# Kernel tuning notes

Hardware: AMD Instinct MI355X
Metric: run time of the kernel (lower is better)

Reference implementation:

```python
import jax, jax.numpy as jnp
import numpy as np

# RosaAttention config constants
H = 16       # num_rosa_heads
KV = 4       # num_rosa_key_value_heads
QKB = 64     # num_rosa_query_key_bits
VB = 64      # num_rosa_value_bits
HID = 2048   # hidden_size
TAU = 1.0    # temperature buffer


def setup_inputs() -> dict:
    key = jax.random.key(0)
    ks = jax.random.split(key, 8)
    B, S = 2, 2048
    sc = 0.02
    return {
        "x": jax.random.normal(ks[0], (B, S, HID), jnp.float32),
        "attention_mask": jnp.ones((B, S), jnp.int32),
        "Wq": jax.random.normal(ks[1], (HID, H * QKB), jnp.float32) * sc,
        "Wk": jax.random.normal(ks[2], (HID, KV * QKB), jnp.float32) * sc,
        "Wv": jax.random.normal(ks[3], (HID, KV * VB), jnp.float32) * sc,
        "Wo": jax.random.normal(ks[4], (H * VB, HID), jnp.float32) * sc,
        "emb0": jnp.full((H, VB), -1e-05, jnp.float32),
        "emb1": jnp.full((H, VB), +1e-05, jnp.float32),
    }


def reference(x, attention_mask, Wq, Wk, Wv, Wo, emb0, emb1):
    B, S, _ = x.shape
    rep = H // KV
    # projections -> [b, s, heads, bits]
    xq = (x @ Wq).reshape(B, S, H, QKB)
    xk = (x @ Wk).reshape(B, S, KV, QKB)
    xv = (x @ Wv).reshape(B, S, KV, VB)
    # repeat_kv: each kv head repeated n_rep times contiguously
    xk = jnp.repeat(xk, rep, axis=2)   # [b, s, H, QKB]
    xv = jnp.repeat(xv, rep, axis=2)   # [b, s, H, VB]
    # soft bit quantization of q/k, tau-scaled bit-similarity score
    qb = jnp.tanh(xq)
    kb = jnp.tanh(xk)
    scores = jnp.einsum('bqhd,bkhd->bhqk', qb, kb) / (TAU * QKB)
    # causal mask + padding mask (mask True = attend)
    causal = jnp.tril(jnp.ones((S, S), bool))
    mask = causal[None, None] & attention_mask.astype(bool)[:, None, None, :]
    scores = jnp.where(mask, scores, jnp.finfo(scores.dtype).min)
    probs = jax.nn.softmax(scores, axis=-1)        # [b, h, q, k]
    # soft-binarized values: per-bit probabilities, attended, then mapped
    # through learned per-head bit embeddings emb0 (bit=0) / emb1 (bit=1)
    vp = jax.nn.sigmoid(xv)                        # [b, s, H, VB]
    ctx = jnp.einsum('bhqk,bkhv->bqhv', probs, vp) # [b, s, H, VB]
    out_bits = ctx * emb1[None, None] + (1.0 - ctx) * emb0[None, None]
    out = out_bits.reshape(B, S, H * VB) @ Wo      # [b, s, HID]
    return out
```

## Files before the change

kernel.cpp:

```cpp
#include <hip/hip_runtime.h>
#include <math.h>

typedef short bf16x8 __attribute__((ext_vector_type(8)));
typedef float f32x4 __attribute__((ext_vector_type(4)));

#define MFMA_BF16(A,B,C) __builtin_amdgcn_mfma_f32_16x16x32_bf16(A,B,C,0,0,0)

__device__ __forceinline__ unsigned short f2b(float x) {
    union { float f; unsigned int u; } v; v.f = x;
    unsigned int r = v.u + 0x7FFFu + ((v.u >> 16) & 1u);
    return (unsigned short)(r >> 16);
}

__device__ __forceinline__ void gload16(const unsigned short* g, unsigned short* l) {
    __builtin_amdgcn_global_load_lds(
        (const __attribute__((address_space(1))) unsigned int*)(g),
        (__attribute__((address_space(3))) unsigned int*)(l),
        16, 0, 0);
}
__device__ __forceinline__ void gload4(const int* g, int* l) {
    __builtin_amdgcn_global_load_lds(
        (const __attribute__((address_space(1))) unsigned int*)(g),
        (__attribute__((address_space(3))) unsigned int*)(l),
        4, 0, 0);
}

__global__ __launch_bounds__(256) void conv_bf16(const float* __restrict__ s,
                                                 unsigned short* __restrict__ d, int n)
{
    int i = blockIdx.x * blockDim.x + threadIdx.x;
    int stride = gridDim.x * blockDim.x;
    for (int idx = i * 4; idx < n; idx += stride * 4) {
        float4 v = *(const float4*)(s + idx);
        ushort4 o;
        o.x = f2b(v.x); o.y = f2b(v.y); o.z = f2b(v.z); o.w = f2b(v.w);
        *(ushort4*)(d + idx) = o;
    }
}

__global__ __launch_bounds__(256) void transp_conv_qkv(const float* __restrict__ Wq,
                                                       const float* __restrict__ Wk,
                                                       const float* __restrict__ Wv,
                                                       unsigned short* __restrict__ dst)
{
    __shared__ float t[32][33];
    const int tx = threadIdx.x, ty = threadIdx.y;
    int bx = blockIdx.x;
    const float* src; int C, cb, dco;
    if (bx < 32)      { src = Wq; C = 1024; cb = bx;      dco = 0; }
    else if (bx < 40) { src = Wk; C = 256;  cb = bx - 32; dco = 1024; }
    else              { src = Wv; C = 256;  cb = bx - 40; dco = 1280; }
    const int c = cb * 32 + tx;
    const int r0 = blockIdx.y * 32;
#pragma unroll
    for (int i = 0; i < 4; ++i)
        t[ty + i * 8][tx] = src[(size_t)(r0 + ty + i * 8) * C + c];
    __syncthreads();
    const int cc = cb * 32 + ty;
#pragma unroll
    for (int i = 0; i < 4; ++i)
        dst[(size_t)(dco + cc + i * 8) * 2048 + r0 + tx] = f2b(t[tx][ty + i * 8]);
}

__global__ __launch_bounds__(256) void transp_conv(const float* __restrict__ src, int R, int C,
                                                   unsigned short* __restrict__ dst, int pitch)
{
    __shared__ float t[32][33];
    const int tx = threadIdx.x, ty = threadIdx.y;
    const int c = blockIdx.x * 32 + tx;
    const int r0 = blockIdx.y * 32;
#pragma unroll
    for (int i = 0; i < 4; ++i)
        t[ty + i * 8][tx] = src[(size_t)(r0 + ty + i * 8) * C + c];
    __syncthreads();
    const int cc = blockIdx.x * 32 + ty;
#pragma unroll
    for (int i = 0; i < 4; ++i)
        dst[(size_t)(cc + i * 8) * pitch + r0 + tx] = f2b(t[tx][ty + i * 8]);
}

template <int MODE>
__global__ __launch_bounds__(256, 3) void gemm_bt_mfma(
    const unsigned short* __restrict__ A,
    const unsigned short* __restrict__ Bt,
    int M, int N, int K,
    float* __restrict__ Cf,
    unsigned short* __restrict__ qh,
    unsigned short* __restrict__ kh,
    unsigned short* __restrict__ vtt)
{
    __shared__ __align__(16) unsigned short As[2][2 * 128 * 32];
    __shared__ __align__(16) unsigned short Bs[2][2 * 64 * 32];

    const int tid = threadIdx.x;
    const int w = tid >> 6, lane = tid & 63, l15 = lane & 15, quad = lane >> 4;
    const int wm = w & 1, wn = w >> 1;
    const int m0 = blockIdx.y * 128, n0 = blockIdx.x * 64;

    f32x4 acc[4][2];
    const f32x4 zero4 = {0.f, 0.f, 0.f, 0.f};
#pragma unroll
    for (int i = 0; i < 4; ++i)
#pragma unroll
        for (int j = 0; j < 2; ++j) acc[i][j] = zero4;

    const int lrow = lane >> 2, lcol = (lane & 3) * 8;
    const unsigned short* AgL = A  + (size_t)(m0 + w * 32 + lrow) * K + lcol;
    const unsigned short* BgL = Bt + (size_t)(n0 + w * 16 + lrow) * K + lcol;

#pragma unroll
    for (int t = 0; t < 4; ++t) {
        const int sub = t >> 1, half = t & 1;
        gload16(AgL + (size_t)(half * 16) * K + sub * 32,
                &As[0][sub * 4096 + (w * 32 + half * 16) * 32]);
    }
#pragma unroll
    for (int kk = 0; kk < 2; ++kk)
        gload16(BgL + kk * 32, &Bs[0][kk * 2048 + (w * 16) * 32]);
    __syncthreads();

    int cb = 0;
    for (int k0 = 0; k0 < K; k0 += 64) {
        if (k0 + 64 < K) {
            const int nb = cb ^ 1;
#pragma unroll
            for (int t = 0; t < 4; ++t) {
                const int sub = t >> 1, half = t & 1;
                gload16(AgL + (size_t)(half * 16) * K + (k0 + 64) + sub * 32,
                        &As[nb][sub * 4096 + (w * 32 + half * 16) * 32]);
            }
#pragma unroll
            for (int kk = 0; kk < 2; ++kk)
                gload16(BgL + (k0 + 64) + kk * 32, &Bs[nb][kk * 2048 + (w * 16) * 32]);
        }

        bf16x8 af[4][2], bf[2][2];
#pragma unroll
        for (int kk = 0; kk < 2; ++kk) {
#pragma unroll
            for (int mt = 0; mt < 4; ++mt)
                af[mt][kk] = *(const bf16x8*)&As[cb][kk * 4096 + (wm * 64 + mt * 16 + l15) * 32 + quad * 8];
#pragma unroll
            for (int nt = 0; nt < 2; ++nt)
                bf[nt][kk] = *(const bf16x8*)&Bs[cb][kk * 2048 + (wn * 32 + nt * 16 + l15) * 32 + quad * 8];
        }
#pragma unroll
        for (int kk = 0; kk < 2; ++kk)
#pragma unroll
            for (int mt = 0; mt < 4; ++mt)
#pragma unroll
                for (int nt = 0; nt < 2; ++nt)
                    acc[mt][nt] = MFMA_BF16(af[mt][kk], bf[nt][kk], acc[mt][nt]);

        __syncthreads();
        cb ^= 1;
    }

    if (MODE == 0) {
#pragma unroll
        for (int mt = 0; mt < 4; ++mt)
#pragma unroll
            for (int nt = 0; nt < 2; ++nt) {
                const int gn = n0 + wn * 32 + nt * 16 + l15;
#pragma unroll
                for (int r = 0; r < 4; ++r) {
                    const int gm = m0 + wm * 64 + mt * 16 + quad * 4 + r;
                    Cf[(size_t)gm * N + gn] = acc[mt][nt][r];
                }
            }
    } else {
        if (n0 < 1024) {
#pragma unroll
            for (int mt = 0; mt < 4; ++mt)
#pragma unroll
                for (int nt = 0; nt < 2; ++nt) {
                    const int gn = n0 + wn * 32 + nt * 16 + l15;
#pragma unroll
                    for (int r = 0; r < 4; ++r) {
                        const int gm = m0 + wm * 64 + mt * 16 + quad * 4 + r;
                        qh[(size_t)gm * 1024 + gn] = f2b(tanhf(acc[mt][nt][r]));
                    }
                }
        } else if (n0 < 1280) {
#pragma unroll
            for (int mt = 0; mt < 4; ++mt)
#pragma unroll
                for (int nt = 0; nt < 2; ++nt) {
                    const int gn = n0 + wn * 32 + nt * 16 + l15 - 1024;
#pragma unroll
                    for (int r = 0; r < 4; ++r) {
                        const int gm = m0 + wm * 64 + mt * 16 + quad * 4 + r;
                        kh[(size_t)gm * 256 + gn] = f2b(tanhf(acc[mt][nt][r]));
                    }
                }
        } else {
#pragma unroll
            for (int mt = 0; mt < 4; ++mt)
#pragma unroll
                for (int nt = 0; nt < 2; ++nt) {
                    const int gn = n0 + wn * 32 + nt * 16 + l15 - 1280;
                    const int g = gn >> 6, vv = gn & 63;
                    const int s0 = m0 + wm * 64 + mt * 16 + quad * 4;
                    const int b = s0 >> 11, sl = s0 & 2047;
                    ushort4 pk;
                    unsigned short* pp = (unsigned short*)&pk;
#pragma unroll
                    for (int r = 0; r < 4; ++r) {
                        float sv = 1.0f / (1.0f + __expf(-acc[mt][nt][r]));
                        pp[r] = f2b(sv);
                    }
                    *(ushort4*)&vtt[((size_t)(b * 4 + g) * 64 + vv) * 2048 + sl] = pk;
                }
        }
    }
}

__global__ __launch_bounds__(256) void rosa_attn_mfma(
    const unsigned short* __restrict__ qh,
    const unsigned short* __restrict__ kh,
    const unsigned short* __restrict__ vtt,
    const int* __restrict__ amask,
    const float* __restrict__ emb0,
    const float* __restrict__ emb1,
    unsigned short* __restrict__ ob)
{
    __shared__ __align__(16) unsigned short Ks[2][2][64 * 32];
    __shared__ __align__(16) unsigned short Vs[2][2][64 * 32];
    __shared__ __align__(16) unsigned short Ps[4][16][72];
    __shared__ int Mski[2][64];

    const int pairI = blockIdx.x;
    const int h = blockIdx.y, b = blockIdx.z, g = h >> 2;
    const int tid = threadIdx.x;
    const int w = tid >> 6, lane = tid & 63, l15 = lane & 15, quad = lane >> 4;

    const int lrow = lane >> 2, lcol = (lane & 3) * 8;
    const unsigned short* kst = kh + (size_t)b * 2048 * 256 + g * 64
                               + (size_t)(w * 16 + lrow) * 256 + lcol;
    const unsigned short* vst = vtt + ((size_t)(b * 4 + g) * 64) * 2048
                               + (size_t)(w * 16 + lrow) * 2048 + lcol;
    const int* mbase = amask + b * 2048;

    const f32x4 zero4 = {0.f, 0.f, 0.f, 0.f};
    const float cexp = 0.0225421100f;

#define STAGE_TILE(k0s, buf)                                              \
    {                                                                     \
        gload16(kst + (size_t)(k0s) * 256,      &Ks[buf][0][(w * 16) * 32]); \
        gload16(kst + (size_t)(k0s) * 256 + 32, &Ks[buf][1][(w * 16) * 32]); \
        gload16(vst + (k0s),                    &Vs[buf][0][(w * 16) * 32]); \
        gload16(vst + (k0s) + 32,               &Vs[buf][1][(w * 16) * 32]); \
        if (w == 0) gload4(mbase + (k0s) + lane, &Mski[buf][0]);          \
    }

    for (int half = 0; half < 2; ++half) {
        const int qt = (half == 0) ? pairI : 31 - pairI;
        const int q0 = qt * 64;
        const int nkt = qt + 1;
        const int qg = q0 + w * 16 + l15;

        const unsigned short* qrow = qh + ((size_t)(b * 2048 + q0 + w * 16 + l15) * 16 + h) * 64;
        const bf16x8 qf0 = *(const bf16x8*)(qrow + quad * 8);
        const bf16x8 qf1 = *(const bf16x8*)(qrow + 32 + quad * 8);

        f32x4 oacc[4];
#pragma unroll
        for (int t = 0; t < 4; ++t) oacc[t] = zero4;
        float psum = 0.0f;

        __syncthreads();
        STAGE_TILE(0, 0)
        __syncthreads();

        int cb = 0;
        for (int kt = 0; kt < nkt; ++kt) {
            if (kt + 1 < nkt) STAGE_TILE((kt + 1) * 64, cb ^ 1)

            const int k0 = kt * 64;
            const bool diag = (kt == qt);
            const int ntlim = diag ? (w + 1) : 4;

#pragma unroll
            for (int nt = 0; nt < 4; ++nt) {
                ushort4 pk;
                if (nt < ntlim) {
                    bf16x8 kf0 = *(const bf16x8*)&Ks[cb][0][(nt * 16 + l15) * 32 + quad * 8];
                    bf16x8 kf1 = *(const bf16x8*)&Ks[cb][1][(nt * 16 + l15) * 32 + quad * 8];
                    f32x4 sc = MFMA_BF16(kf0, qf0, zero4);
                    sc = MFMA_BF16(kf1, qf1, sc);
                    const int4 m4 = *(const int4*)&Mski[cb][nt * 16 + quad * 4];
                    const int* mm = (const int*)&m4;
                    unsigned short* pp = (unsigned short*)&pk;
#pragma unroll
                    for (int r = 0; r < 4; ++r) {
                        float p = __builtin_exp2f(sc[r] * cexp);
                        bool valid = (mm[r] != 0);
                        if (diag) valid = valid && ((k0 + nt * 16 + quad * 4 + r) <= qg);
                        p = valid ? p : 0.0f;
                        psum += p;
                        pp[r] = f2b(p);
                    }
                } else {
                    pk.x = 0; pk.y = 0; pk.z = 0; pk.w = 0;
                }
                *(ushort4*)&Ps[w][l15][nt * 16 + quad * 4] = pk;
            }

            const bf16x8 pf0 = *(const bf16x8*)&Ps[w][l15][quad * 8];
            const bf16x8 pf1 = *(const bf16x8*)&Ps[w][l15][32 + quad * 8];
#pragma unroll
            for (int nt = 0; nt < 4; ++nt) {
                bf16x8 vf0 = *(const bf16x8*)&Vs[cb][0][(nt * 16 + l15) * 32 + quad * 8];
                bf16x8 vf1 = *(const bf16x8*)&Vs[cb][1][(nt * 16 + l15) * 32 + quad * 8];
                oacc[nt] = MFMA_BF16(pf0, vf0, oacc[nt]);
                oacc[nt] = MFMA_BF16(pf1, vf1, oacc[nt]);
            }

            if (kt + 1 < nkt) {
                __syncthreads();
                cb ^= 1;
            }
        }

        float l = psum;
        l += __shfl_xor(l, 16);
        l += __shfl_xor(l, 32);
        float lq[4];
#pragma unroll
        for (int r = 0; r < 4; ++r) lq[r] = __shfl(l, quad * 4 + r);

#pragma unroll
        for (int nt = 0; nt < 4; ++nt) {
            const float e0 = emb0[h * 64 + nt * 16 + l15];
            const float e1 = emb1[h * 64 + nt * 16 + l15];
#pragma unroll
            for (int r = 0; r < 4; ++r) {
                const float ctx = oacc[nt][r] / lq[r];
                const float val = e0 + ctx * (e1 - e0);
                const size_t s_idx = (size_t)(b * 2048 + q0 + w * 16 + quad * 4 + r);
                ob[(s_idx * 16 + h) * 64 + nt * 16 + l15] = f2b(val);
            }
        }
    }
#undef STAGE_TILE
}

extern "C" void kernel_launch(void* const* d_in, const int* in_sizes, int n_in,
                              void* d_out, int out_size, void* d_ws, size_t ws_size,
                              hipStream_t stream)
{
    const float* x    = (const float*)d_in[0];
    const int*   amask= (const int*)d_in[1];
    const float* Wq   = (const float*)d_in[2];
    const float* Wk   = (const float*)d_in[3];
    const float* Wv   = (const float*)d_in[4];
    const float* Wo   = (const float*)d_in[5];
    const float* emb0 = (const float*)d_in[6];
    const float* emb1 = (const float*)d_in[7];
    float* out = (float*)d_out;

    char* base = (char*)d_ws;
    unsigned short* xh    = (unsigned short*)(base);
    unsigned short* ob    = xh;
    unsigned short* Wqkvt = (unsigned short*)(base + (16u << 20));
    unsigned short* Wot   = (unsigned short*)(base + (22u << 20));
    unsigned short* qh    = (unsigned short*)(base + (26u << 20));
    unsigned short* kh    = (unsigned short*)(base + (34u << 20));
    unsigned short* vtt   = (unsigned short*)(base + (36u << 20));

    conv_bf16<<<2048, 256, 0, stream>>>(x, xh, 4096 * 2048);
    transp_conv_qkv<<<dim3(48, 64), dim3(32, 8), 0, stream>>>(Wq, Wk, Wv, Wqkvt);
    transp_conv<<<dim3(64, 32), dim3(32, 8), 0, stream>>>(Wo, 1024, 2048, Wot, 1024);

    gemm_bt_mfma<1><<<dim3(24, 32), 256, 0, stream>>>(xh, Wqkvt, 4096, 1536, 2048,
                                                      nullptr, qh, kh, vtt);
    rosa_attn_mfma<<<dim3(16, 16, 2), 256, 0, stream>>>(qh, kh, vtt, amask, emb0, emb1, ob);
    gemm_bt_mfma<0><<<dim3(32, 32), 256, 0, stream>>>(ob, Wot, 4096, 2048, 1024,
                                                      out, nullptr, nullptr, nullptr);
}
```

Baseline: 234.7 us.

## Share K/V tiles across both paired query tiles in one key loop

The attention kernel used to run two separate key loops, one per query tile in the causal pair, and reloaded K/V tiles for each. Now a single loop over the longer tile's keys stages each K/V tile once. Both query tiles are computed from register-cached K and V fragments, with the short tile active only while kt <= qt0. This cuts global and LDS traffic for K/V and the number of barriers. In exchange it needs more registers for two accumulator sets and the cached fragments, which may lower occupancy.

```diff
diff --git a/kernel.cpp b/kernel.cpp
--- a/kernel.cpp
+++ b/kernel.cpp
@@ -226,13 +226,18 @@
 {
     __shared__ __align__(16) unsigned short Ks[2][2][64 * 32];
     __shared__ __align__(16) unsigned short Vs[2][2][64 * 32];
-    __shared__ __align__(16) unsigned short Ps[4][16][72];
+    __shared__ __align__(16) unsigned short Ps[4][2][16][72];
     __shared__ int Mski[2][64];
 
     const int pairI = blockIdx.x;
     const int h = blockIdx.y, b = blockIdx.z, g = h >> 2;
     const int tid = threadIdx.x;
     const int w = tid >> 6, lane = tid & 63, l15 = lane & 15, quad = lane >> 4;
+
+    const int qt0 = pairI, qt1 = 31 - pairI;
+    const int q00 = qt0 * 64, q01 = qt1 * 64;
+    const int qg0 = q00 + w * 16 + l15;
+    const int qg1 = q01 + w * 16 + l15;
 
     const int lrow = lane >> 2, lcol = (lane & 3) * 8;
     const unsigned short* kst = kh + (size_t)b * 2048 * 256 + g * 64
@@ -243,6 +248,18 @@
 
     const f32x4 zero4 = {0.f, 0.f, 0.f, 0.f};
     const float cexp = 0.0225421100f;
+
+    const unsigned short* qrow0 = qh + ((size_t)(b * 2048 + q00 + w * 16 + l15) * 16 + h) * 64;
+    const unsigned short* qrow1 = qh + ((size_t)(b * 2048 + q01 + w * 16 + l15) * 16 + h) * 64;
+    const bf16x8 qf00 = *(const bf16x8*)(qrow0 + quad * 8);
+    const bf16x8 qf01 = *(const bf16x8*)(qrow0 + 32 + quad * 8);
+    const bf16x8 qf10 = *(const bf16x8*)(qrow1 + quad * 8);
+    const bf16x8 qf11 = *(const bf16x8*)(qrow1 + 32 + quad * 8);
+
+    f32x4 oacc0[4], oacc1[4];
+#pragma unroll
+    for (int t = 0; t < 4; ++t) { oacc0[t] = zero4; oacc1[t] = zero4; }
+    float psum0 = 0.0f, psum1 = 0.0f;
 
 #define STAGE_TILE(k0s, buf)                                              \
     {                                                                     \
@@ -253,41 +270,34 @@
         if (w == 0) gload4(mbase + (k0s) + lane, &Mski[buf][0]);          \
     }
 
-    for (int half = 0; half < 2; ++half) {
-        const int qt = (half == 0) ? pairI : 31 - pairI;
-        const int q0 = qt * 64;
-        const int nkt = qt + 1;
-        const int qg = q0 + w * 16 + l15;
-
-        const unsigned short* qrow = qh + ((size_t)(b * 2048 + q0 + w * 16 + l15) * 16 + h) * 64;
-        const bf16x8 qf0 = *(const bf16x8*)(qrow + quad * 8);
-        const bf16x8 qf1 = *(const bf16x8*)(qrow + 32 + quad * 8);
-
-        f32x4 oacc[4];
-#pragma unroll
-        for (int t = 0; t < 4; ++t) oacc[t] = zero4;
-        float psum = 0.0f;
-
-        __syncthreads();
-        STAGE_TILE(0, 0)
-        __syncthreads();
-
-        int cb = 0;
-        for (int kt = 0; kt < nkt; ++kt) {
-            if (kt + 1 < nkt) STAGE_TILE((kt + 1) * 64, cb ^ 1)
-
-            const int k0 = kt * 64;
-            const bool diag = (kt == qt);
+    STAGE_TILE(0, 0)
+    __syncthreads();
+
+    int cb = 0;
+    const int nkt = qt1 + 1;
+    for (int kt = 0; kt < nkt; ++kt) {
+        if (kt + 1 < nkt) STAGE_TILE((kt + 1) * 64, cb ^ 1)
+
+        const int k0 = kt * 64;
+
+        bf16x8 kf[4][2], vf[4][2];
+#pragma unroll
+        for (int nt = 0; nt < 4; ++nt) {
+            kf[nt][0] = *(const bf16x8*)&Ks[cb][0][(nt * 16 + l15) * 32 + quad * 8];
+            kf[nt][1] = *(const bf16x8*)&Ks[cb][1][(nt * 16 + l15) * 32 + quad * 8];
+            vf[nt][0] = *(const bf16x8*)&Vs[cb][0][(nt * 16 + l15) * 32 + quad * 8];
+            vf[nt][1] = *(const bf16x8*)&Vs[cb][1][(nt * 16 + l15) * 32 + quad * 8];
+        }
+
+        if (kt <= qt0) {
+            const bool diag = (kt == qt0);
             const int ntlim = diag ? (w + 1) : 4;
-
 #pragma unroll
             for (int nt = 0; nt < 4; ++nt) {
                 ushort4 pk;
                 if (nt < ntlim) {
-                    bf16x8 kf0 = *(const bf16x8*)&Ks[cb][0][(nt * 16 + l15) * 32 + quad * 8];
-                    bf16x8 kf1 = *(const bf16x8*)&Ks[cb][1][(nt * 16 + l15) * 32 + quad * 8];
-                    f32x4 sc = MFMA_BF16(kf0, qf0, zero4);
-                    sc = MFMA_BF16(kf1, qf1, sc);
+                    f32x4 sc = MFMA_BF16(kf[nt][0], qf00, zero4);
+                    sc = MFMA_BF16(kf[nt][1], qf01, sc);
                     const int4 m4 = *(const int4*)&Mski[cb][nt * 16 + quad * 4];
                     const int* mm = (const int*)&m4;
                     unsigned short* pp = (unsigned short*)&pk;
@@ -295,32 +305,72 @@
                     for (int r = 0; r < 4; ++r) {
                         float p = __builtin_exp2f(sc[r] * cexp);
                         bool valid = (mm[r] != 0);
-                        if (diag) valid = valid && ((k0 + nt * 16 + quad * 4 + r) <= qg);
+                        if (diag) valid = valid && ((k0 + nt * 16 + quad * 4 + r) <= qg0);
                         p = valid ? p : 0.0f;
-                        psum += p;
+                        psum0 += p;
                         pp[r] = f2b(p);
                     }
                 } else {
                     pk.x = 0; pk.y = 0; pk.z = 0; pk.w = 0;
                 }
-                *(ushort4*)&Ps[w][l15][nt * 16 + quad * 4] = pk;
-            }
-
-            const bf16x8 pf0 = *(const bf16x8*)&Ps[w][l15][quad * 8];
-            const bf16x8 pf1 = *(const bf16x8*)&Ps[w][l15][32 + quad * 8];
+                *(ushort4*)&Ps[w][0][l15][nt * 16 + quad * 4] = pk;
+            }
+            const bf16x8 pf0 = *(const bf16x8*)&Ps[w][0][l15][quad * 8];
+            const bf16x8 pf1 = *(const bf16x8*)&Ps[w][0][l15][32 + quad * 8];
 #pragma unroll
             for (int nt = 0; nt < 4; ++nt) {
-                bf16x8 vf0 = *(const bf16x8*)&Vs[cb][0][(nt * 16 + l15) * 32 + quad * 8];
-                bf16x8 vf1 = *(const bf16x8*)&Vs[cb][1][(nt * 16 + l15) * 32 + quad * 8];
-                oacc[nt] = MFMA_BF16(pf0, vf0, oacc[nt]);
-                oacc[nt] = MFMA_BF16(pf1, vf1, oacc[nt]);
-            }
-
-            if (kt + 1 < nkt) {
-                __syncthreads();
-                cb ^= 1;
-            }
-        }
+                oacc0[nt] = MFMA_BF16(pf0, vf[nt][0], oacc0[nt]);
+                oacc0[nt] = MFMA_BF16(pf1, vf[nt][1], oacc0[nt]);
+            }
+        }
+
+        {
+            const bool diag = (kt == qt1);
+            const int ntlim = diag ? (w + 1) : 4;
+#pragma unroll
+            for (int nt = 0; nt < 4; ++nt) {
+                ushort4 pk;
+                if (nt < ntlim) {
+                    f32x4 sc = MFMA_BF16(kf[nt][0], qf10, zero4);
+                    sc = MFMA_BF16(kf[nt][1], qf11, sc);
+                    const int4 m4 = *(const int4*)&Mski[cb][nt * 16 + quad * 4];
+                    const int* mm = (const int*)&m4;
+                    unsigned short* pp = (unsigned short*)&pk;
+#pragma unroll
+                    for (int r = 0; r < 4; ++r) {
+                        float p = __builtin_exp2f(sc[r] * cexp);
+                        bool valid = (mm[r] != 0);
+                        if (diag) valid = valid && ((k0 + nt * 16 + quad * 4 + r) <= qg1);
+                        p = valid ? p : 0.0f;
+                        psum1 += p;
+                        pp[r] = f2b(p);
+                    }
+                } else {
+                    pk.x = 0; pk.y = 0; pk.z = 0; pk.w = 0;
+                }
+                *(ushort4*)&Ps[w][1][l15][nt * 16 + quad * 4] = pk;
+            }
+            const bf16x8 pf0 = *(const bf16x8*)&Ps[w][1][l15][quad * 8];
+            const bf16x8 pf1 = *(const bf16x8*)&Ps[w][1][l15][32 + quad * 8];
+#pragma unroll
+            for (int nt = 0; nt < 4; ++nt) {
+                oacc1[nt] = MFMA_BF16(pf0, vf[nt][0], oacc1[nt]);
+                oacc1[nt] = MFMA_BF16(pf1, vf[nt][1], oacc1[nt]);
+            }
+        }
+
+        if (kt + 1 < nkt) {
+            __syncthreads();
+            cb ^= 1;
+        }
+    }
+#undef STAGE_TILE
+
+#pragma unroll
+    for (int half = 0; half < 2; ++half) {
+        const float psum = half ? psum1 : psum0;
+        const int q0 = half ? q01 : q00;
+        f32x4* oacc = half ? oacc1 : oacc0;
 
         float l = psum;
         l += __shfl_xor(l, 16);
@@ -342,7 +392,6 @@
             }
         }
     }
-#undef STAGE_TILE
 }
 
 extern "C" void kernel_launch(void* const* d_in, const int* in_sizes, int n_in,
```

Result: no change. 239.4 us (+2.0%).
